# Performance work log

Measured on AMD Instinct MI355X. Metric: run time of the kernel, lower is better.

The kernel has to match this reference:

```python
import jax, jax.numpy as jnp
import numpy as np

B, V, J = 16384, 8, 21  # batch, views, joints (J=21 hard-coded in LAT)


def setup_inputs() -> dict:
    key = jax.random.key(0)
    k1, k2, k3, k4 = jax.random.split(key, 4)
    intrinsic = jax.random.normal(k1, (B, V, 3, 3), dtype=jnp.float32)
    extrinsic = jax.random.normal(k2, (B, V, 3, 4), dtype=jnp.float32)
    # uv ~ pixel coordinates in [0, 256)
    uv = jax.random.uniform(k3, (B, V, J, 2), dtype=jnp.float32) * 256.0
    confidences = jax.random.uniform(k4, (B, V, J), dtype=jnp.float32)
    return {"intrinsic": intrinsic, "extrinsic": extrinsic, "uv": uv,
            "confidences": confidences}


def reference(intrinsic, extrinsic, uv, confidences):
    # Projection matrices P = K @ [R|T]: (B,V,3,4)
    P = jnp.einsum('bvij,bvjk->bvik', intrinsic, extrinsic)
    Pj = P[:, :, None]                      # (B,V,1,3,4), broadcast over joints
    u = uv[..., 0:1]                        # (B,V,J,1)
    v = uv[..., 1:2]                        # (B,V,J,1)
    w = confidences[..., None]              # (B,V,J,1)
    # Weighted DLT rows: (B,V,J,4)
    row0 = w * (u * Pj[..., 2, :] - Pj[..., 0, :])
    row1 = w * (v * Pj[..., 2, :] - Pj[..., 1, :])
    A = jnp.stack([row0, row1], axis=3)     # (B,V,J,2,4)
    A = A.transpose(0, 2, 1, 3, 4).reshape(B * J, 2 * V, 4)  # (BJ, 2V, 4)
    # Smallest right singular vector of each (2V,4) system
    _, _, Vh = jnp.linalg.svd(A, full_matrices=False)  # Vh: (BJ,4,4)
    X_homo = Vh[:, -1, :]                   # (BJ, 4)
    w_homo = X_homo[:, 3:4]                 # (BJ, 1)
    total_w = confidences.sum(axis=1).reshape(B * J, 1)
    valid = ((total_w > 0.1) & (jnp.abs(w_homo) > 1e-6)).astype(X_homo.dtype)
    X_3d = X_homo[:, :3] / (w_homo + 1e-8) * valid
    return X_3d.reshape(B, J, 3)
```

## Files before the change

kernel.cpp:

```cpp
#include <hip/hip_runtime.h>
#include <math.h>

constexpr int B = 16384;
constexpr int V = 8;
constexpr int J = 21;


__device__ __forceinline__ double fast_rsqrt(double u) {
    double r = (double)__builtin_amdgcn_rsqf((float)u);
    double hu = -0.5 * u;
    r = r * fma(hu * r, r, 1.5);
    r = r * fma(hu * r, r, 1.5);
    return r;
}

#define JROT(app, aqq, apq, ar0p, ar0q, ar1p, ar1q,                        \
             v0p, v0q, v1p, v1q, v2p, v2q, v3p, v3q)                       \
  {                                                                        \
    double d_ = aqq - app;                                                 \
    double u1_ = fma(d_, d_, 4.0 * (apq * apq));                           \
    double rinv_ = fast_rsqrt(u1_);                                        \
    double c2_ = fma(0.5 * fabs(d_), rinv_, 0.5);                          \
    double invc_ = fast_rsqrt(c2_);                                        \
    double c_ = c2_ * invc_;                                               \
    double s_ = ((d_ >= 0.0) ? apq : -apq) * (rinv_ * invc_);              \
    double t_ = s_ * invc_;                                                \
    bool z_ = (apq == 0.0);                                                \
    c_ = z_ ? 1.0 : c_;                                                    \
    s_ = z_ ? 0.0 : s_;                                                    \
    t_ = z_ ? 0.0 : t_;                                                    \
    double tapq_ = t_ * apq;                                               \
    app -= tapq_;                                                          \
    aqq += tapq_;                                                          \
    apq = 0.0;                                                             \
    double x_, y_;                                                         \
    x_ = ar0p; y_ = ar0q;                                                  \
    ar0p = fma(c_, x_, -s_ * y_); ar0q = fma(s_, x_, c_ * y_);             \
    x_ = ar1p; y_ = ar1q;                                                  \
    ar1p = fma(c_, x_, -s_ * y_); ar1q = fma(s_, x_, c_ * y_);             \
    x_ = v0p; y_ = v0q;                                                    \
    v0p = fma(c_, x_, -s_ * y_); v0q = fma(s_, x_, c_ * y_);               \
    x_ = v1p; y_ = v1q;                                                    \
    v1p = fma(c_, x_, -s_ * y_); v1q = fma(s_, x_, c_ * y_);               \
    x_ = v2p; y_ = v2q;                                                    \
    v2p = fma(c_, x_, -s_ * y_); v2q = fma(s_, x_, c_ * y_);               \
    x_ = v3p; y_ = v3q;                                                    \
    v3p = fma(c_, x_, -s_ * y_); v3q = fma(s_, x_, c_ * y_);               \
  }

__global__ __launch_bounds__(64, 4)
void triangulate_kernel(const float* __restrict__ intr,
                        const float* __restrict__ extr,
                        const float* __restrict__ uv,
                        const float* __restrict__ conf,
                        float* __restrict__ out)
{
    int t = blockIdx.x * blockDim.x + threadIdx.x;
    if (t >= B * J) return;
    int b = t / J;
    int j = t - b * J;

    double m00 = 0, m01 = 0, m02 = 0, m03 = 0;
    double m11 = 0, m12 = 0, m13 = 0;
    double m22 = 0, m23 = 0;
    double m33 = 0;
    float total_w = 0.0f;

    for (int v = 0; v < V; ++v) {
        const float* Kp = intr + (size_t)(b * V + v) * 9;
        const float* Ep = extr + (size_t)(b * V + v) * 12;
        float K0 = Kp[0], K1 = Kp[1], K2 = Kp[2];
        float K3 = Kp[3], K4 = Kp[4], K5 = Kp[5];
        float K6 = Kp[6], K7 = Kp[7], K8 = Kp[8];

        float P0[4], P1[4], P2[4];
        #pragma unroll
        for (int k = 0; k < 4; ++k) {
            float e0 = Ep[k], e1 = Ep[4 + k], e2 = Ep[8 + k];
            P0[k] = fmaf(K0, e0, fmaf(K1, e1, __fmul_rn(K2, e2)));
            P1[k] = fmaf(K3, e0, fmaf(K4, e1, __fmul_rn(K5, e2)));
            P2[k] = fmaf(K6, e0, fmaf(K7, e1, __fmul_rn(K8, e2)));
        }

        size_t uvbase = (size_t)(b * V + v) * J + j;
        float uu = uv[uvbase * 2 + 0];
        float vv = uv[uvbase * 2 + 1];
        float w  = conf[uvbase];
        total_w += w;

        float r0[4], r1[4];
        #pragma unroll
        for (int k = 0; k < 4; ++k) {
            r0[k] = __fmul_rn(w, fmaf(uu, P2[k], -P0[k]));
            r1[k] = __fmul_rn(w, fmaf(vv, P2[k], -P1[k]));
        }

        m00 += (double)r0[0] * r0[0] + (double)r1[0] * r1[0];
        m01 += (double)r0[0] * r0[1] + (double)r1[0] * r1[1];
        m02 += (double)r0[0] * r0[2] + (double)r1[0] * r1[2];
        m03 += (double)r0[0] * r0[3] + (double)r1[0] * r1[3];
        m11 += (double)r0[1] * r0[1] + (double)r1[1] * r1[1];
        m12 += (double)r0[1] * r0[2] + (double)r1[1] * r1[2];
        m13 += (double)r0[1] * r0[3] + (double)r1[1] * r1[3];
        m22 += (double)r0[2] * r0[2] + (double)r1[2] * r1[2];
        m23 += (double)r0[2] * r0[3] + (double)r1[2] * r1[3];
        m33 += (double)r0[3] * r0[3] + (double)r1[3] * r1[3];
    }

    double v00 = 1, v01 = 0, v02 = 0, v03 = 0;
    double v10 = 0, v11 = 1, v12 = 0, v13 = 0;
    double v20 = 0, v21 = 0, v22 = 1, v23 = 0;
    double v30 = 0, v31 = 0, v32 = 0, v33 = 1;

    for (int sweep = 0; sweep < 8; ++sweep) {
        JROT(m00, m11, m01,  m02, m12,  m03, m13,
             v00, v01, v10, v11, v20, v21, v30, v31);
        JROT(m00, m22, m02,  m01, m12,  m03, m23,
             v00, v02, v10, v12, v20, v22, v30, v32);
        JROT(m00, m33, m03,  m01, m13,  m02, m23,
             v00, v03, v10, v13, v20, v23, v30, v33);
        JROT(m11, m22, m12,  m01, m02,  m13, m23,
             v01, v02, v11, v12, v21, v22, v31, v32);
        JROT(m11, m33, m13,  m01, m03,  m12, m23,
             v01, v03, v11, v13, v21, v23, v31, v33);
        JROT(m22, m33, m23,  m02, m03,  m12, m13,
             v02, v03, v12, v13, v22, v23, v32, v33);

        double off2 = m01*m01 + m02*m02 + m03*m03
                    + m12*m12 + m13*m13 + m23*m23;
        double tr = m00 + m11 + m22 + m33;
        if (__all(off2 <= 1e-30 * tr * tr)) break;
    }

    double be = m00;
    double x0 = v00, x1 = v10, x2 = v20, x3 = v30;
    if (m11 < be) { be = m11; x0 = v01; x1 = v11; x2 = v21; x3 = v31; }
    if (m22 < be) { be = m22; x0 = v02; x1 = v12; x2 = v22; x3 = v32; }
    if (m33 < be) { be = m33; x0 = v03; x1 = v13; x2 = v23; x3 = v33; }

    float xw = (float)x3;
    bool valid = (total_w > 0.1f) && (fabsf(xw) > 1e-6f);
    float denom = xw + 1e-8f;
    float o0 = valid ? (float)x0 / denom : 0.0f;
    float o1 = valid ? (float)x1 / denom : 0.0f;
    float o2 = valid ? (float)x2 / denom : 0.0f;

    out[(size_t)t * 3 + 0] = o0;
    out[(size_t)t * 3 + 1] = o1;
    out[(size_t)t * 3 + 2] = o2;
}

extern "C" void kernel_launch(void* const* d_in, const int* in_sizes, int n_in,
                              void* d_out, int out_size, void* d_ws, size_t ws_size,
                              hipStream_t stream) {
    const float* intr = (const float*)d_in[0];
    const float* extr = (const float*)d_in[1];
    const float* uv   = (const float*)d_in[2];
    const float* conf = (const float*)d_in[3];
    float* out = (float*)d_out;

    int total = B * J;
    int block = 64;
    int grid = (total + block - 1) / block;
    triangulate_kernel<<<grid, block, 0, stream>>>(intr, extr, uv, conf, out);
}
```

Measured before the change: 39.80 us.

## Use parallel-ordering Jacobi stages and cut Newton refinement and tolerance

```diff
diff --git a/kernel.cpp b/kernel.cpp
--- a/kernel.cpp
+++ b/kernel.cpp
@@ -10,42 +10,49 @@
     double r = (double)__builtin_amdgcn_rsqf((float)u);
     double hu = -0.5 * u;
     r = r * fma(hu * r, r, 1.5);
-    r = r * fma(hu * r, r, 1.5);
     return r;
 }
 
-#define JROT(app, aqq, apq, ar0p, ar0q, ar1p, ar1q,                        \
-             v0p, v0q, v1p, v1q, v2p, v2q, v3p, v3q)                       \
+#define PSTAGE(app, aqq, apq, arr, ass, ars, ca, cb, cd, ce,               \
+               v0p, v0q, v1p, v1q, v2p, v2q, v3p, v3q,                     \
+               w0r, w0s, w1r, w1s, w2r, w2s, w3r, w3s)                     \
   {                                                                        \
-    double d_ = aqq - app;                                                 \
-    double u1_ = fma(d_, d_, 4.0 * (apq * apq));                           \
-    double rinv_ = fast_rsqrt(u1_);                                        \
-    double c2_ = fma(0.5 * fabs(d_), rinv_, 0.5);                          \
-    double invc_ = fast_rsqrt(c2_);                                        \
-    double c_ = c2_ * invc_;                                               \
-    double s_ = ((d_ >= 0.0) ? apq : -apq) * (rinv_ * invc_);              \
-    double t_ = s_ * invc_;                                                \
-    bool z_ = (apq == 0.0);                                                \
-    c_ = z_ ? 1.0 : c_;                                                    \
-    s_ = z_ ? 0.0 : s_;                                                    \
-    t_ = z_ ? 0.0 : t_;                                                    \
-    double tapq_ = t_ * apq;                                               \
-    app -= tapq_;                                                          \
-    aqq += tapq_;                                                          \
-    apq = 0.0;                                                             \
+    double dA_ = aqq - app;                                                \
+    double uA_ = fma(dA_, dA_, 4.0 * (apq * apq));                         \
+    double riA_ = fast_rsqrt(uA_);                                         \
+    double c2A_ = fma(0.5 * fabs(dA_), riA_, 0.5);                         \
+    double icA_ = fast_rsqrt(c2A_);                                        \
+    double cA_ = c2A_ * icA_;                                              \
+    double sA_ = ((dA_ >= 0.0) ? apq : -apq) * (riA_ * icA_);              \
+    double tA_ = sA_ * icA_;                                               \
+    bool zA_ = (apq == 0.0);                                               \
+    cA_ = zA_ ? 1.0 : cA_; sA_ = zA_ ? 0.0 : sA_; tA_ = zA_ ? 0.0 : tA_;   \
+    double dB_ = ass - arr;                                                \
+    double uB_ = fma(dB_, dB_, 4.0 * (ars * ars));                         \
+    double riB_ = fast_rsqrt(uB_);                                         \
+    double c2B_ = fma(0.5 * fabs(dB_), riB_, 0.5);                         \
+    double icB_ = fast_rsqrt(c2B_);                                        \
+    double cB_ = c2B_ * icB_;                                              \
+    double sB_ = ((dB_ >= 0.0) ? ars : -ars) * (riB_ * icB_);              \
+    double tB_ = sB_ * icB_;                                               \
+    bool zB_ = (ars == 0.0);                                               \
+    cB_ = zB_ ? 1.0 : cB_; sB_ = zB_ ? 0.0 : sB_; tB_ = zB_ ? 0.0 : tB_;   \
+    double tpA_ = tA_ * apq; app -= tpA_; aqq += tpA_; apq = 0.0;          \
+    double tpB_ = tB_ * ars; arr -= tpB_; ass += tpB_; ars = 0.0;          \
+    double a_ = ca, b_ = cb, d_ = cd, e_ = ce;                             \
+    double a1_ = fma(cA_, a_, -sA_ * d_), d1_ = fma(sA_, a_, cA_ * d_);    \
+    double b1_ = fma(cA_, b_, -sA_ * e_), e1_ = fma(sA_, b_, cA_ * e_);    \
+    ca = fma(cB_, a1_, -sB_ * b1_); cb = fma(sB_, a1_, cB_ * b1_);         \
+    cd = fma(cB_, d1_, -sB_ * e1_); ce = fma(sB_, d1_, cB_ * e1_);         \
     double x_, y_;                                                         \
-    x_ = ar0p; y_ = ar0q;                                                  \
-    ar0p = fma(c_, x_, -s_ * y_); ar0q = fma(s_, x_, c_ * y_);             \
-    x_ = ar1p; y_ = ar1q;                                                  \
-    ar1p = fma(c_, x_, -s_ * y_); ar1q = fma(s_, x_, c_ * y_);             \
-    x_ = v0p; y_ = v0q;                                                    \
-    v0p = fma(c_, x_, -s_ * y_); v0q = fma(s_, x_, c_ * y_);               \
-    x_ = v1p; y_ = v1q;                                                    \
-    v1p = fma(c_, x_, -s_ * y_); v1q = fma(s_, x_, c_ * y_);               \
-    x_ = v2p; y_ = v2q;                                                    \
-    v2p = fma(c_, x_, -s_ * y_); v2q = fma(s_, x_, c_ * y_);               \
-    x_ = v3p; y_ = v3q;                                                    \
-    v3p = fma(c_, x_, -s_ * y_); v3q = fma(s_, x_, c_ * y_);               \
+    x_ = v0p; y_ = v0q; v0p = fma(cA_, x_, -sA_ * y_); v0q = fma(sA_, x_, cA_ * y_); \
+    x_ = v1p; y_ = v1q; v1p = fma(cA_, x_, -sA_ * y_); v1q = fma(sA_, x_, cA_ * y_); \
+    x_ = v2p; y_ = v2q; v2p = fma(cA_, x_, -sA_ * y_); v2q = fma(sA_, x_, cA_ * y_); \
+    x_ = v3p; y_ = v3q; v3p = fma(cA_, x_, -sA_ * y_); v3q = fma(sA_, x_, cA_ * y_); \
+    x_ = w0r; y_ = w0s; w0r = fma(cB_, x_, -sB_ * y_); w0s = fma(sB_, x_, cB_ * y_); \
+    x_ = w1r; y_ = w1s; w1r = fma(cB_, x_, -sB_ * y_); w1s = fma(sB_, x_, cB_ * y_); \
+    x_ = w2r; y_ = w2s; w2r = fma(cB_, x_, -sB_ * y_); w2s = fma(sB_, x_, cB_ * y_); \
+    x_ = w3r; y_ = w3s; w3r = fma(cB_, x_, -sB_ * y_); w3s = fma(sB_, x_, cB_ * y_); \
   }
 
 __global__ __launch_bounds__(64, 4)
@@ -113,23 +120,20 @@
     double v30 = 0, v31 = 0, v32 = 0, v33 = 1;
 
     for (int sweep = 0; sweep < 8; ++sweep) {
-        JROT(m00, m11, m01,  m02, m12,  m03, m13,
-             v00, v01, v10, v11, v20, v21, v30, v31);
-        JROT(m00, m22, m02,  m01, m12,  m03, m23,
-             v00, v02, v10, v12, v20, v22, v30, v32);
-        JROT(m00, m33, m03,  m01, m13,  m02, m23,
-             v00, v03, v10, v13, v20, v23, v30, v33);
-        JROT(m11, m22, m12,  m01, m02,  m13, m23,
-             v01, v02, v11, v12, v21, v22, v31, v32);
-        JROT(m11, m33, m13,  m01, m03,  m12, m23,
-             v01, v03, v11, v13, v21, v23, v31, v33);
-        JROT(m22, m33, m23,  m02, m03,  m12, m13,
-             v02, v03, v12, v13, v22, v23, v32, v33);
+        PSTAGE(m00, m11, m01,  m22, m33, m23,  m02, m03, m12, m13,
+               v00, v01, v10, v11, v20, v21, v30, v31,
+               v02, v03, v12, v13, v22, v23, v32, v33);
+        PSTAGE(m00, m22, m02,  m11, m33, m13,  m01, m03, m12, m23,
+               v00, v02, v10, v12, v20, v22, v30, v32,
+               v01, v03, v11, v13, v21, v23, v31, v33);
+        PSTAGE(m00, m33, m03,  m11, m22, m12,  m01, m02, m13, m23,
+               v00, v03, v10, v13, v20, v23, v30, v33,
+               v01, v02, v11, v12, v21, v22, v31, v32);
 
         double off2 = m01*m01 + m02*m02 + m03*m03
                     + m12*m12 + m13*m13 + m23*m23;
         double tr = m00 + m11 + m22 + m33;
-        if (__all(off2 <= 1e-30 * tr * tr)) break;
+        if (__all(off2 <= 1e-26 * tr * tr)) break;
     }
 
     double be = m00;
```

Measured after the change: 35.54 us. 10.7% less time.
